# Optimization experiments

Measured on AMD Instinct MI355X. Metric: run time of the kernel, lower is better.

The kernel has to match this reference:

```python
import jax, jax.numpy as jnp
import numpy as np

RESERVOIR_SIZE = 2048
EMBED = 768
N_FRAMES = 256
NUM_CLASSES = 1000
BATCH = 128
SPARSITY = 0.05
SPECTRAL_RADIUS = 0.8


def _init_reservoir(key):
    k1, k2 = jax.random.split(key)
    w = jax.random.normal(k1, (RESERVOIR_SIZE, RESERVOIR_SIZE), dtype=jnp.float32)
    mask = (jax.random.uniform(k2, (RESERVOIR_SIZE, RESERVOIR_SIZE)) < SPARSITY).astype(jnp.float32)
    r = w * mask
    # rescale so spectral radius == SPECTRAL_RADIUS (matches torch eigvals-based init)
    eig = np.linalg.eigvals(np.asarray(r))
    max_abs = np.abs(eig).max()
    return r * (SPECTRAL_RADIUS / jnp.float32(max_abs))


def setup_inputs() -> dict:
    key = jax.random.key(0)
    kx, kr, kin, kout = jax.random.split(key, 4)
    x = jax.random.normal(kx, (BATCH, N_FRAMES, EMBED), dtype=jnp.float32)
    reservoir = _init_reservoir(kr)
    W_in = jax.random.normal(kin, (RESERVOIR_SIZE, EMBED), dtype=jnp.float32) * 0.1
    W_out = jax.random.normal(kout, (NUM_CLASSES, RESERVOIR_SIZE), dtype=jnp.float32) * 0.02
    b_out = jnp.zeros((NUM_CLASSES,), dtype=jnp.float32)
    return {"x": x, "reservoir": reservoir, "W_in": W_in, "W_out": W_out, "b_out": b_out}


def reference(x, reservoir, W_in, W_out, b_out):
    # x: [B, T, E]. Precompute input projections for all frames in one GEMM:
    # u[t] = x[:, t] @ W_in.T  -> [T, B, R]
    u = jnp.einsum("bte,re->tbr", x, W_in)
    state0 = jnp.zeros((x.shape[0], reservoir.shape[0]), dtype=x.dtype)

    def step(state, u_t):
        new_state = jnp.tanh(state @ reservoir.T + u_t)
        return new_state, None

    state, _ = jax.lax.scan(step, state0, u)
    # linear head (dropout is identity in eval mode)
    logits = state @ W_out.T + b_out
    return logits
```

## Files before the change

### kernel.cpp

```cpp
#include <hip/hip_runtime.h>
#include <stdint.h>
#include <stddef.h>

#define BATCH 128
#define NFRAMES 256
#define EMBED 768
#define RES 2048
#define NCLS 1000
#define NWG 256

typedef __attribute__((ext_vector_type(8))) short bf16x8;
typedef __attribute__((ext_vector_type(4))) float f32x4;
typedef unsigned short u16;

__device__ inline u16 f2bf(float f) {
    union { float f; unsigned u; } v; v.f = f;
    unsigned r = v.u + 0x7FFFu + ((v.u >> 16) & 1u);
    return (u16)(r >> 16);
}
__device__ inline float tanh_fast(float x) {
    float z = __builtin_amdgcn_exp2f(x * 2.885390081777927f);
    return 1.f - 2.f * __builtin_amdgcn_rcpf(z + 1.f);
}

__global__ __launch_bounds__(256) void cvt_kernel(const float* __restrict__ in,
                                                  u16* __restrict__ out, int n4) {
    int i = blockIdx.x * blockDim.x + threadIdx.x;
    int stride = gridDim.x * blockDim.x;
    for (; i < n4; i += stride) {
        float4 v = ((const float4*)in)[i];
        ushort4 o;
        o.x = f2bf(v.x); o.y = f2bf(v.y); o.z = f2bf(v.z); o.w = f2bf(v.w);
        ((ushort4*)out)[i] = o;
    }
}

__global__ __launch_bounds__(512, 1) void recur_kernel(const u16* __restrict__ res,
                                                       const u16* __restrict__ win,
                                                       const u16* __restrict__ xb,
                                                       u16* __restrict__ ring,
                                                       const u16* __restrict__ s0,
                                                       unsigned* __restrict__ flags) {
    __shared__ float part[2][8][16][66];
    __shared__ unsigned cnt;
    const int lane = threadIdx.x & 63;
    const int w = threadIdx.x >> 6;
    const int rowgrp = (int)(blockIdx.x & 7);
    const int colblk = (int)(blockIdx.x >> 3);
    const int m0 = rowgrp * 16;
    const int n0 = colblk * 64;
    const int lr = lane & 15;
    const int lk = (lane >> 4) * 8;
    const int rb = (lane >> 4) * 4;
    const int kbase = w * 256;
    const int xkbase = w * 96;
    unsigned* myflag = flags + rowgrp * 32 + colblk;
    const unsigned* pollflag = flags + rowgrp * 32 + (lane & 31);

    if (threadIdx.x == 0) cnt = 0;

    bf16x8 bfr[4][8];
#pragma unroll
    for (int jf = 0; jf < 4; jf++)
#pragma unroll
        for (int kk = 0; kk < 8; kk++)
            bfr[jf][kk] = *(const bf16x8*)(res + (size_t)(n0 + jf * 16 + lr) * RES + kbase + kk * 32 + lk);

    bf16x8 wfr[4][3];
#pragma unroll
    for (int jf = 0; jf < 4; jf++)
#pragma unroll
        for (int j = 0; j < 3; j++)
            wfr[jf][j] = *(const bf16x8*)(win + (size_t)(n0 + jf * 16 + lr) * EMBED + xkbase + j * 32 + lk);

    const int er = threadIdx.x >> 5;
    const int ec = (threadIdx.x & 31) * 2;
    const size_t gidx = (size_t)(m0 + er) * RES + n0 + ec;
    const u16* xrow = xb + (size_t)(m0 + lr) * NFRAMES * EMBED + xkbase + lk;

    f32x4 xacc[4];
#pragma unroll
    for (int jf = 0; jf < 4; jf++) xacc[jf] = (f32x4)0.f;
    {
        bf16x8 xa[3];
#pragma unroll
        for (int j = 0; j < 3; j++)
            asm volatile("global_load_dwordx4 %0, %1, off"
                         : "=v"(xa[j]) : "v"(xrow + j * 32));
        asm volatile("s_waitcnt vmcnt(0)" ::: "memory");
        __builtin_amdgcn_sched_barrier(0);
#pragma unroll
        for (int j = 0; j < 3; j++)
#pragma unroll
            for (int jf = 0; jf < 4; jf++)
                xacc[jf] = __builtin_amdgcn_mfma_f32_16x16x32_bf16(xa[j], wfr[jf][j], xacc[jf], 0, 0, 0);
    }

    for (int t = 0; t < NFRAMES; t++) {
        const u16* sin = (t == 0) ? s0 : ring + (size_t)(t - 1) * BATCH * RES;
        u16* sout = ring + (size_t)t * BATCH * RES;
        const u16* abase = sin + (size_t)(m0 + lr) * RES + kbase + lk;
        const int cur = t & 1;

        if (t > 0) {
            if (w == 0) {
                unsigned f;
                do {
                    asm volatile("global_load_dword %0, %1, off sc0 sc1\n\ts_waitcnt vmcnt(0)"
                                 : "=v"(f) : "v"(pollflag) : "memory");
                    if (__all((int)(f >= (unsigned)t))) break;
                    __builtin_amdgcn_s_sleep(1);
                } while (1);
            }
            __syncthreads();
        }

        bf16x8 a[8];
#pragma unroll
        for (int kk = 0; kk < 8; kk++)
            asm volatile("global_load_dwordx4 %0, %1, off"
                         : "=v"(a[kk]) : "v"(abase + kk * 32));

        f32x4 acc[4];
#pragma unroll
        for (int jf = 0; jf < 4; jf++) acc[jf] = xacc[jf];

        asm volatile("s_waitcnt vmcnt(4)" ::: "memory");
        __builtin_amdgcn_sched_barrier(0);
#pragma unroll
        for (int kk = 0; kk < 4; kk++)
#pragma unroll
            for (int jf = 0; jf < 4; jf++)
                acc[jf] = __builtin_amdgcn_mfma_f32_16x16x32_bf16(a[kk], bfr[jf][kk], acc[jf], 0, 0, 0);
        asm volatile("s_waitcnt vmcnt(0)" ::: "memory");
        __builtin_amdgcn_sched_barrier(0);
#pragma unroll
        for (int kk = 4; kk < 8; kk++)
#pragma unroll
            for (int jf = 0; jf < 4; jf++)
                acc[jf] = __builtin_amdgcn_mfma_f32_16x16x32_bf16(a[kk], bfr[jf][kk], acc[jf], 0, 0, 0);

#pragma unroll
        for (int jf = 0; jf < 4; jf++)
#pragma unroll
            for (int q = 0; q < 4; q++)
                part[cur][w][rb + q][jf * 16 + lr] = acc[jf][q];
        __syncthreads();

        float sx = 0.f, sy = 0.f;
#pragma unroll
        for (int ww = 0; ww < 8; ww++) {
            float2 v = *(const float2*)&part[cur][ww][er][ec];
            sx += v.x; sy += v.y;
        }
        float v0 = tanh_fast(sx);
        float v1 = tanh_fast(sy);
        unsigned pk = (unsigned)f2bf(v0) | ((unsigned)f2bf(v1) << 16);
        asm volatile("global_store_dword %0, %1, off sc0 sc1"
                     :: "v"(sout + gidx), "v"(pk) : "memory");

        asm volatile("s_waitcnt vmcnt(0)" ::: "memory");
        if (t != NFRAMES - 1) {
            if (lane == 0) {
                unsigned old = atomicAdd(&cnt, 1u);
                if (old == (unsigned)(8 * t + 7)) {
                    unsigned stamp = (unsigned)(t + 1);
                    asm volatile("global_store_dword %0, %1, off sc0 sc1"
                                 :: "v"(myflag), "v"(stamp) : "memory");
                }
            }
            const u16* xp = xrow + (size_t)(t + 1) * EMBED;
            bf16x8 xa[3];
#pragma unroll
            for (int j = 0; j < 3; j++)
                asm volatile("global_load_dwordx4 %0, %1, off"
                             : "=v"(xa[j]) : "v"(xp + j * 32));
#pragma unroll
            for (int jf = 0; jf < 4; jf++) xacc[jf] = (f32x4)0.f;
            asm volatile("s_waitcnt vmcnt(0)" ::: "memory");
            __builtin_amdgcn_sched_barrier(0);
#pragma unroll
            for (int j = 0; j < 3; j++)
#pragma unroll
                for (int jf = 0; jf < 4; jf++)
                    xacc[jf] = __builtin_amdgcn_mfma_f32_16x16x32_bf16(xa[j], wfr[jf][j], xacc[jf], 0, 0, 0);
        }
    }
}

__global__ __launch_bounds__(512) void head_kernel(const u16* __restrict__ sin,
                                                   const u16* __restrict__ wout,
                                                   const float* __restrict__ bias,
                                                   float* __restrict__ out) {
    __shared__ float part[8][32][33];
    int lane = threadIdx.x & 63;
    int w = threadIdx.x >> 6;
    int m0 = blockIdx.x * 32;
    int n0 = blockIdx.y * 32;
    int k0 = w * 256;
    int lr = lane & 15;
    int lk = (lane >> 4) * 8;

    f32x4 acc[2][2];
#pragma unroll
    for (int i = 0; i < 2; i++)
#pragma unroll
        for (int j = 0; j < 2; j++) acc[i][j] = (f32x4)0.f;

    for (int kk = k0; kk < k0 + 256; kk += 32) {
        bf16x8 a[2], b[2];
#pragma unroll
        for (int i = 0; i < 2; i++)
            a[i] = *(const bf16x8*)(sin + (size_t)(m0 + i * 16 + lr) * RES + kk + lk);
#pragma unroll
        for (int j = 0; j < 2; j++) {
            int row = n0 + j * 16 + lr;
            if (row > NCLS - 1) row = NCLS - 1;
            b[j] = *(const bf16x8*)(wout + (size_t)row * RES + kk + lk);
        }
#pragma unroll
        for (int i = 0; i < 2; i++)
#pragma unroll
            for (int j = 0; j < 2; j++)
                acc[i][j] = __builtin_amdgcn_mfma_f32_16x16x32_bf16(a[i], b[j], acc[i][j], 0, 0, 0);
    }

    int rowbase = (lane >> 4) * 4;
#pragma unroll
    for (int i = 0; i < 2; i++)
#pragma unroll
        for (int j = 0; j < 2; j++)
#pragma unroll
            for (int q = 0; q < 4; q++)
                part[w][i * 16 + rowbase + q][j * 16 + lr] = acc[i][j][q];

    __syncthreads();

    for (int idx = threadIdx.x; idx < 1024; idx += 512) {
        int r = idx >> 5, c = idx & 31;
        float s = 0.f;
#pragma unroll
        for (int ww = 0; ww < 8; ww++) s += part[ww][r][c];
        int cg = n0 + c;
        if (cg < NCLS)
            out[(size_t)(m0 + r) * NCLS + cg] = s + bias[cg];
    }
}

extern "C" void kernel_launch(void* const* d_in, const int* in_sizes, int n_in,
                              void* d_out, int out_size, void* d_ws, size_t ws_size,
                              hipStream_t stream) {
    const float* x_f    = (const float*)d_in[0];
    const float* res_f  = (const float*)d_in[1];
    const float* win_f  = (const float*)d_in[2];
    const float* wout_f = (const float*)d_in[3];
    const float* bias   = (const float*)d_in[4];
    float* out = (float*)d_out;

    char* ws = (char*)d_ws;
    size_t off = 0;
    auto alloc = [&](size_t bytes) -> void* {
        void* p = ws + off;
        off += (bytes + 255) & ~(size_t)255;
        return p;
    };
    u16* res_b  = (u16*)alloc((size_t)RES * RES * 2);
    u16* win_b  = (u16*)alloc((size_t)RES * EMBED * 2);
    u16* wout_b = (u16*)alloc((size_t)NCLS * RES * 2);
    u16* x_b    = (u16*)alloc((size_t)BATCH * NFRAMES * EMBED * 2);
    u16* ring   = (u16*)alloc((size_t)NFRAMES * BATCH * RES * 2);
    u16* s0     = (u16*)alloc((size_t)BATCH * RES * 2);
    unsigned* flags = (unsigned*)alloc(1024);

    cvt_kernel<<<dim3(1024), dim3(256), 0, stream>>>(res_f, res_b, RES * RES / 4);
    cvt_kernel<<<dim3(512), dim3(256), 0, stream>>>(win_f, win_b, RES * EMBED / 4);
    cvt_kernel<<<dim3(512), dim3(256), 0, stream>>>(wout_f, wout_b, NCLS * RES / 4);
    cvt_kernel<<<dim3(2048), dim3(256), 0, stream>>>(x_f, x_b, BATCH * NFRAMES * EMBED / 4);

    hipMemsetAsync(s0, 0, (size_t)BATCH * RES * 2, stream);
    hipMemsetAsync(flags, 0, 1024, stream);

    void* args[] = { (void*)&res_b, (void*)&win_b, (void*)&x_b, (void*)&ring,
                     (void*)&s0, (void*)&flags };
    hipLaunchCooperativeKernel((const void*)recur_kernel, dim3(NWG), dim3(512),
                               args, 0, stream);

    const u16* sfin = ring + (size_t)(NFRAMES - 1) * BATCH * RES;
    head_kernel<<<dim3(4, 32), dim3(512), 0, stream>>>(sfin, wout_b, bias, out);
}
```

Measured before the change: 1.132 ms.

## Replace per-step global barrier with per-chunk dataflow waits in recurrence

Each wave now waits only for the four producer column blocks whose state slices it consumes, instead of all 32, and processes each 64-wide K chunk as soon as its flag is set. Wave 0 polls the global flags and publishes them to a shared chunkstamp array that other waves spin on. The input projection MFMA for the next step is deferred to the start of the step so it overlaps the wait. This trades the block-wide barrier for finer-grained polling, more LDS traffic and serialized load-then-wait per chunk, which may lower memory-level parallelism.

```diff
diff --git a/kernel.cpp b/kernel.cpp
--- a/kernel.cpp
+++ b/kernel.cpp
@@ -35,6 +35,20 @@
     }
 }
 
+#define PROC_CHUNK(j) do {                                                        \
+    bf16x8 a0_, a1_;                                                              \
+    asm volatile("global_load_dwordx4 %0, %1, off" : "=v"(a0_) : "v"(abase + (j)*64));      \
+    asm volatile("global_load_dwordx4 %0, %1, off" : "=v"(a1_) : "v"(abase + (j)*64 + 32)); \
+    asm volatile("s_waitcnt vmcnt(0)" ::: "memory");                              \
+    __builtin_amdgcn_sched_barrier(0);                                            \
+    _Pragma("unroll")                                                             \
+    for (int jf_ = 0; jf_ < 4; jf_++)                                             \
+        acc[jf_] = __builtin_amdgcn_mfma_f32_16x16x32_bf16(a0_, bfr[jf_][2*(j)], acc[jf_], 0, 0, 0);   \
+    _Pragma("unroll")                                                             \
+    for (int jf_ = 0; jf_ < 4; jf_++)                                             \
+        acc[jf_] = __builtin_amdgcn_mfma_f32_16x16x32_bf16(a1_, bfr[jf_][2*(j)+1], acc[jf_], 0, 0, 0); \
+} while (0)
+
 __global__ __launch_bounds__(512, 1) void recur_kernel(const u16* __restrict__ res,
                                                        const u16* __restrict__ win,
                                                        const u16* __restrict__ xb,
@@ -42,6 +56,7 @@
                                                        const u16* __restrict__ s0,
                                                        unsigned* __restrict__ flags) {
     __shared__ float part[2][8][16][66];
+    __shared__ unsigned chunkstamp[32];
     __shared__ unsigned cnt;
     const int lane = threadIdx.x & 63;
     const int w = threadIdx.x >> 6;
@@ -58,6 +73,7 @@
     const unsigned* pollflag = flags + rowgrp * 32 + (lane & 31);
 
     if (threadIdx.x == 0) cnt = 0;
+    if (threadIdx.x < 32) ((volatile unsigned*)chunkstamp)[threadIdx.x] = 0;
 
     bf16x8 bfr[4][8];
 #pragma unroll
@@ -78,23 +94,13 @@
     const size_t gidx = (size_t)(m0 + er) * RES + n0 + ec;
     const u16* xrow = xb + (size_t)(m0 + lr) * NFRAMES * EMBED + xkbase + lk;
 
-    f32x4 xacc[4];
-#pragma unroll
-    for (int jf = 0; jf < 4; jf++) xacc[jf] = (f32x4)0.f;
-    {
-        bf16x8 xa[3];
-#pragma unroll
-        for (int j = 0; j < 3; j++)
-            asm volatile("global_load_dwordx4 %0, %1, off"
-                         : "=v"(xa[j]) : "v"(xrow + j * 32));
-        asm volatile("s_waitcnt vmcnt(0)" ::: "memory");
-        __builtin_amdgcn_sched_barrier(0);
-#pragma unroll
-        for (int j = 0; j < 3; j++)
-#pragma unroll
-            for (int jf = 0; jf < 4; jf++)
-                xacc[jf] = __builtin_amdgcn_mfma_f32_16x16x32_bf16(xa[j], wfr[jf][j], xacc[jf], 0, 0, 0);
-    }
+    __syncthreads();
+
+    bf16x8 xa[3];
+#pragma unroll
+    for (int j = 0; j < 3; j++)
+        asm volatile("global_load_dwordx4 %0, %1, off"
+                     : "=v"(xa[j]) : "v"(xrow + j * 32));
 
     for (int t = 0; t < NFRAMES; t++) {
         const u16* sin = (t == 0) ? s0 : ring + (size_t)(t - 1) * BATCH * RES;
@@ -102,43 +108,55 @@
         const u16* abase = sin + (size_t)(m0 + lr) * RES + kbase + lk;
         const int cur = t & 1;
 
-        if (t > 0) {
-            if (w == 0) {
-                unsigned f;
-                do {
-                    asm volatile("global_load_dword %0, %1, off sc0 sc1\n\ts_waitcnt vmcnt(0)"
-                                 : "=v"(f) : "v"(pollflag) : "memory");
-                    if (__all((int)(f >= (unsigned)t))) break;
-                    __builtin_amdgcn_s_sleep(1);
-                } while (1);
-            }
-            __syncthreads();
-        }
-
-        bf16x8 a[8];
-#pragma unroll
-        for (int kk = 0; kk < 8; kk++)
-            asm volatile("global_load_dwordx4 %0, %1, off"
-                         : "=v"(a[kk]) : "v"(abase + kk * 32));
-
         f32x4 acc[4];
 #pragma unroll
-        for (int jf = 0; jf < 4; jf++) acc[jf] = xacc[jf];
-
-        asm volatile("s_waitcnt vmcnt(4)" ::: "memory");
-        __builtin_amdgcn_sched_barrier(0);
-#pragma unroll
-        for (int kk = 0; kk < 4; kk++)
-#pragma unroll
-            for (int jf = 0; jf < 4; jf++)
-                acc[jf] = __builtin_amdgcn_mfma_f32_16x16x32_bf16(a[kk], bfr[jf][kk], acc[jf], 0, 0, 0);
+        for (int jf = 0; jf < 4; jf++) acc[jf] = (f32x4)0.f;
         asm volatile("s_waitcnt vmcnt(0)" ::: "memory");
         __builtin_amdgcn_sched_barrier(0);
 #pragma unroll
-        for (int kk = 4; kk < 8; kk++)
+        for (int j = 0; j < 3; j++)
 #pragma unroll
             for (int jf = 0; jf < 4; jf++)
-                acc[jf] = __builtin_amdgcn_mfma_f32_16x16x32_bf16(a[kk], bfr[jf][kk], acc[jf], 0, 0, 0);
+                acc[jf] = __builtin_amdgcn_mfma_f32_16x16x32_bf16(xa[j], wfr[jf][j], acc[jf], 0, 0, 0);
+
+        if (t == 0) {
+            PROC_CHUNK(0); PROC_CHUNK(1); PROC_CHUNK(2); PROC_CHUNK(3);
+        } else if (w == 0) {
+            unsigned done = 0;
+            while (1) {
+                unsigned f;
+                asm volatile("global_load_dword %0, %1, off sc0 sc1\n\ts_waitcnt vmcnt(0)"
+                             : "=v"(f) : "v"(pollflag) : "memory");
+                if (lane < 32) ((volatile unsigned*)chunkstamp)[lane] = f;
+#pragma unroll
+                for (int j = 0; j < 4; j++) {
+                    unsigned fj = __shfl(f, j, 64);
+                    if (!((done >> j) & 1u) && fj >= (unsigned)t) {
+                        PROC_CHUNK(j);
+                        done |= 1u << j;
+                    }
+                }
+                if (__all((int)(f >= (unsigned)t))) break;
+                __builtin_amdgcn_s_sleep(1);
+            }
+        } else {
+            unsigned done = 0;
+            while (done != 0xFu) {
+                bool prog = false;
+#pragma unroll
+                for (int j = 0; j < 4; j++) {
+                    if (!((done >> j) & 1u)) {
+                        unsigned s = ((volatile unsigned*)chunkstamp)[4 * w + j];
+                        if (s >= (unsigned)t) {
+                            PROC_CHUNK(j);
+                            done |= 1u << j;
+                            prog = true;
+                        }
+                    }
+                }
+                if (done != 0xFu && !prog) __builtin_amdgcn_s_sleep(1);
+            }
+        }
 
 #pragma unroll
         for (int jf = 0; jf < 4; jf++)
@@ -170,20 +188,10 @@
                 }
             }
             const u16* xp = xrow + (size_t)(t + 1) * EMBED;
-            bf16x8 xa[3];
 #pragma unroll
             for (int j = 0; j < 3; j++)
                 asm volatile("global_load_dwordx4 %0, %1, off"
                              : "=v"(xa[j]) : "v"(xp + j * 32));
-#pragma unroll
-            for (int jf = 0; jf < 4; jf++) xacc[jf] = (f32x4)0.f;
-            asm volatile("s_waitcnt vmcnt(0)" ::: "memory");
-            __builtin_amdgcn_sched_barrier(0);
-#pragma unroll
-            for (int j = 0; j < 3; j++)
-#pragma unroll
-                for (int jf = 0; jf < 4; jf++)
-                    xacc[jf] = __builtin_amdgcn_mfma_f32_16x16x32_bf16(xa[j], wfr[jf][j], xacc[jf], 0, 0, 0);
         }
     }
 }
```

New measurement: 1.330 ms. 17.6% more time.
